# Kernel optimization log

Hardware: AMD Instinct MI355X
Metric: run time of the kernel (lower is better)

Reference implementation:

```python
import jax, jax.numpy as jnp
import numpy as np
import math

B, S, IN_DIM, OUT_DIM = 16, 1024, 512, 256
THETA = 10000.0


def _rope_single(x, cos, sin):
    # x: [B,S,D]; cos/sin: [D//2] -- SAME rotation applied at every position
    # (faithful to original: freqs_cis[seq_len*2] selects a single row)
    xr = x.reshape(x.shape[0], x.shape[1], -1, 2)
    a, b = xr[..., 0], xr[..., 1]
    out = jnp.stack([a * cos - b * sin, a * sin + b * cos], axis=-1)
    return out.reshape(x.shape)


def setup_inputs() -> dict:
    key = jax.random.key(0)
    ks = jax.random.split(key, 4)
    scale = 1.0 / math.sqrt(IN_DIM)
    x = jax.random.normal(ks[0], (B, S, IN_DIM), jnp.float32)
    wq = jax.random.normal(ks[1], (OUT_DIM, IN_DIM), jnp.float32) * scale
    wk = jax.random.normal(ks[2], (OUT_DIM, IN_DIM), jnp.float32) * scale
    wv = jax.random.normal(ks[3], (OUT_DIM, IN_DIM), jnp.float32) * scale
    bq = jnp.zeros((OUT_DIM,), jnp.float32)
    bk = jnp.zeros((OUT_DIM,), jnp.float32)
    bv = jnp.zeros((OUT_DIM,), jnp.float32)
    return {"x": x, "wq": wq, "bq": bq, "wk": wk, "bk": bk, "wv": wv, "bv": bv}


def reference(x, wq, bq, wk, bk, wv, bv):
    dim = x.shape[-1]  # scale uses INPUT dim, per original code
    # freqs_cis row at position index = 2*seq_len
    inv_freq = 1.0 / (THETA ** (jnp.arange(0, OUT_DIM, 2, dtype=jnp.float32) / OUT_DIM))
    angle = (2.0 * S) * inv_freq  # [OUT_DIM//2]
    cos, sin = jnp.cos(angle), jnp.sin(angle)

    q = jnp.einsum('bsi,oi->bso', x, wq) + bq
    k = jnp.einsum('bsi,oi->bso', x, wk) + bk
    v = jnp.einsum('bsi,oi->bso', x, wv) + bv

    q = _rope_single(q, cos, sin)
    k = _rope_single(k, cos, sin)

    scores = jnp.einsum('bqd,bkd->bqk', q, k) / jnp.sqrt(jnp.float32(dim))
    scores = jax.nn.softmax(scores.astype(jnp.float32), axis=-1)
    out = jnp.einsum('bqk,bkd->bqd', scores, v)
    return out
```

## Files before the change

### kernel.cpp

```cpp
#include <hip/hip_runtime.h>
#include <hip/hip_bf16.h>


typedef __attribute__((ext_vector_type(8))) short short8;
typedef __attribute__((ext_vector_type(4))) short short4v;
typedef __attribute__((ext_vector_type(4))) float f32x4;

#define GLL16(g, l)                                                            \
  __builtin_amdgcn_global_load_lds(                                            \
      (const __attribute__((address_space(1))) unsigned int*)(g),              \
      (__attribute__((address_space(3))) unsigned int*)(l), 16, 0, 0)

static __device__ __forceinline__ short f2bf(float f) {
  __hip_bfloat16 h = __float2bfloat16(f);
  return __builtin_bit_cast(short, h);
}

__global__ __launch_bounds__(256) void qkv_gemm(
    const float* __restrict__ x, const float* __restrict__ wq,
    const float* __restrict__ wk, const float* __restrict__ wv,
    const float* __restrict__ bq, const float* __restrict__ bk,
    const float* __restrict__ bv, short* __restrict__ qb,
    short* __restrict__ kb, short* __restrict__ vt) {
  __shared__ __align__(16) char smem[32768];
  const int bid = blockIdx.x;
  const int swz = (bid & 7) * 96 + (bid >> 3);
  const int mt = swz / 6, nt = swz % 6;
  const int tid = threadIdx.x;
  const int w = tid >> 6, lane = tid & 63;
  const int g = lane >> 4, c = lane & 15;
  const int wm = w >> 1, wn = w & 1;

  const float* wsel = (nt < 2) ? wq : (nt < 4) ? wk : wv;
  const int wro = (nt & 1) * 128;

  f32x4 acc[4][4];
  const f32x4 fzero = {0.f, 0.f, 0.f, 0.f};
#pragma unroll
  for (int mi = 0; mi < 4; mi++)
#pragma unroll
    for (int ni = 0; ni < 4; ni++) acc[mi][ni] = fzero;

  const int arow = tid >> 4;
  const int acol4 = tid & 15;
  const int achunk = acol4 >> 1, ahalf = (tid & 1) * 8;

  for (int kk = 0; kk < 8; ++kk) {
    __syncthreads();
    float4 xv[8], wv8[8];
#pragma unroll
    for (int j = 0; j < 8; j++) {
      int row = j * 16 + arow;
      xv[j] = *(const float4*)(x + (mt * 128 + row) * 512 + kk * 64 + acol4 * 4);
    }
#pragma unroll
    for (int j = 0; j < 8; j++) {
      int row = j * 16 + arow;
      wv8[j] = *(const float4*)(wsel + (wro + row) * 512 + kk * 64 + acol4 * 4);
    }
#pragma unroll
    for (int j = 0; j < 8; j++) {
      int row = j * 16 + arow;
      short4v s4;
      s4[0] = f2bf(xv[j].x); s4[1] = f2bf(xv[j].y);
      s4[2] = f2bf(xv[j].z); s4[3] = f2bf(xv[j].w);
      *(short4v*)(smem + row * 128 + ((achunk ^ (row & 7)) * 16) + ahalf) = s4;
      short4v t4;
      t4[0] = f2bf(wv8[j].x); t4[1] = f2bf(wv8[j].y);
      t4[2] = f2bf(wv8[j].z); t4[3] = f2bf(wv8[j].w);
      *(short4v*)(smem + 16384 + row * 128 + ((achunk ^ (row & 7)) * 16) + ahalf) = t4;
    }
    __syncthreads();
#pragma unroll
    for (int ks = 0; ks < 2; ++ks) {
      short8 af[4], bf[4];
#pragma unroll
      for (int mi = 0; mi < 4; mi++) {
        int row = wm * 64 + mi * 16 + c;
        af[mi] = *(const short8*)(smem + row * 128 + (((ks * 4 + g) ^ (row & 7)) * 16));
      }
#pragma unroll
      for (int ni = 0; ni < 4; ni++) {
        int row = wn * 64 + ni * 16 + c;
        bf[ni] = *(const short8*)(smem + 16384 + row * 128 + (((ks * 4 + g) ^ (row & 7)) * 16));
      }
#pragma unroll
      for (int mi = 0; mi < 4; mi++)
#pragma unroll
        for (int ni = 0; ni < 4; ni++)
          acc[mi][ni] = __builtin_amdgcn_mfma_f32_16x16x32_bf16(af[mi], bf[ni], acc[mi][ni], 0, 0, 0);
    }
  }

  const int cls = nt >> 1;
  const int cw = (nt & 1) * 128 + wn * 64;
  const int rowbase = mt * 128 + wm * 64;
  if (cls == 0) {
#pragma unroll
    for (int ni = 0; ni < 4; ni++) {
      int col = cw + ni * 16 + c;
      float bias = bq[col];
#pragma unroll
      for (int mi = 0; mi < 4; mi++)
#pragma unroll
        for (int j = 0; j < 4; j++) {
          int row = rowbase + mi * 16 + g * 4 + j;
          qb[row * 256 + col] = f2bf((acc[mi][ni][j] + bias) * 0.044194173824159216f);
        }
    }
  } else if (cls == 1) {
#pragma unroll
    for (int ni = 0; ni < 4; ni++) {
      int col = cw + ni * 16 + c;
      float bias = bk[col];
#pragma unroll
      for (int mi = 0; mi < 4; mi++)
#pragma unroll
        for (int j = 0; j < 4; j++) {
          int row = rowbase + mi * 16 + g * 4 + j;
          kb[row * 256 + col] = f2bf(acc[mi][ni][j] + bias);
        }
    }
  } else {
    __syncthreads();
    char* tb = smem + w * 8192;
#pragma unroll
    for (int ni = 0; ni < 4; ni++) {
      int dl = ni * 16 + c;
      float bias = bv[cw + dl];
#pragma unroll
      for (int mi = 0; mi < 4; mi++)
#pragma unroll
        for (int j = 0; j < 4; j++) {
          int sl = mi * 16 + g * 4 + j;
          *(short*)(tb + dl * 128 + ((sl * 2) ^ ((dl & 7) << 4))) =
              f2bf(acc[mi][ni][j] + bias);
        }
    }
    const int bb = rowbase >> 10, sb = rowbase & 1023;
#pragma unroll
    for (int i = 0; i < 8; i++) {
      int dl = i * 8 + (lane >> 3);
      int ch = lane & 7;
      short8 val = *(const short8*)(tb + dl * 128 + ((ch ^ (dl & 7)) * 16));
      *(short8*)(vt + (bb * 256 + cw + dl) * 1024 + sb + ch * 8) = val;
    }
  }
}

__global__ __launch_bounds__(512) void attn_kernel(
    const short* __restrict__ qb, const short* __restrict__ kb,
    const short* __restrict__ vt, float* __restrict__ out) {
  __shared__ __align__(16) char smem[149504];
  const int bid = blockIdx.x;
  const int swz = (bid & 7) * 32 + (bid >> 3);
  const int b = swz >> 4, qt = swz & 15;
  const int tid = threadIdx.x;
  const int w = tid >> 6, lane = tid & 63;
  const int grp = w >> 2, lw = w & 3;
  const int g = lane >> 4, c = lane & 15;
  const int q0 = b * 1024 + qt * 64 + lw * 16;
  char* kbase = smem + grp * 32768;
  char* vbase = smem + 65536 + grp * 32768;
  short* sp = (short*)(smem + 131072 + w * 2304);

  short8 qf[8];
#pragma unroll
  for (int ks = 0; ks < 8; ks++)
    qf[ks] = *(const short8*)(qb + (q0 + c) * 256 + ks * 32 + g * 8);

  f32x4 O[16];
  const f32x4 fzero = {0.f, 0.f, 0.f, 0.f};
#pragma unroll
  for (int ni = 0; ni < 16; ni++) O[ni] = fzero;
  float m_[4] = {-1e30f, -1e30f, -1e30f, -1e30f};
  float l_[4] = {0.f, 0.f, 0.f, 0.f};

  const int krow0 = b * 1024 + grp * 512;

  for (int kt = 0; kt < 8; ++kt) {
    __syncthreads();
    if (lw < 2) {
#pragma unroll
      for (int i = 0; i < 16; i++) {
        int j = lw * 16 + i;
        int r = j * 2 + (lane >> 5);
        int cc = lane & 31;
        GLL16(kb + (krow0 + kt * 64 + r) * 256 + ((cc ^ (r & 7)) * 8),
              kbase + j * 1024);
      }
    } else {
#pragma unroll
      for (int i = 0; i < 16; i++) {
        int j = (lw - 2) * 16 + i;
        int r = j * 8 + (lane >> 3);
        int cc = lane & 7;
        GLL16(vt + (b * 256 + r) * 1024 + grp * 512 + kt * 64 + ((cc ^ (r & 7)) * 8),
              vbase + j * 1024);
      }
    }
    asm volatile("s_waitcnt vmcnt(0)" ::: "memory");
    __syncthreads();

    f32x4 Sf[4];
#pragma unroll
    for (int nf = 0; nf < 4; nf++) Sf[nf] = fzero;
#pragma unroll
    for (int ks = 0; ks < 8; ks++) {
      short8 kf[4];
#pragma unroll
      for (int nf = 0; nf < 4; nf++) {
        int key = nf * 16 + c;
        kf[nf] = *(const short8*)(kbase + key * 512 + (((ks * 4 + g) ^ (c & 7)) * 16));
      }
#pragma unroll
      for (int nf = 0; nf < 4; nf++)
        Sf[nf] = __builtin_amdgcn_mfma_f32_16x16x32_bf16(qf[ks], kf[nf], Sf[nf], 0, 0, 0);
    }

    float Pv[4][4], scl[4];
#pragma unroll
    for (int j = 0; j < 4; j++) {
      float tm = fmaxf(fmaxf(Sf[0][j], Sf[1][j]), fmaxf(Sf[2][j], Sf[3][j]));
      tm = fmaxf(tm, __shfl_xor(tm, 1));
      tm = fmaxf(tm, __shfl_xor(tm, 2));
      tm = fmaxf(tm, __shfl_xor(tm, 4));
      tm = fmaxf(tm, __shfl_xor(tm, 8));
      float nm = fmaxf(m_[j], tm);
      scl[j] = __expf(m_[j] - nm);
      m_[j] = nm;
      float rs = 0.f;
#pragma unroll
      for (int nf = 0; nf < 4; nf++) {
        float p = __expf(Sf[nf][j] - nm);
        Pv[nf][j] = p;
        rs += p;
      }
      rs += __shfl_xor(rs, 1);
      rs += __shfl_xor(rs, 2);
      rs += __shfl_xor(rs, 4);
      rs += __shfl_xor(rs, 8);
      l_[j] = l_[j] * scl[j] + rs;
    }
#pragma unroll
    for (int ni = 0; ni < 16; ni++) {
      O[ni][0] *= scl[0]; O[ni][1] *= scl[1];
      O[ni][2] *= scl[2]; O[ni][3] *= scl[3];
    }

#pragma unroll
    for (int nf = 0; nf < 4; nf++)
#pragma unroll
      for (int j = 0; j < 4; j++)
        sp[(g * 4 + j) * 72 + nf * 16 + c] = f2bf(Pv[nf][j]);

    short8 pf[2];
#pragma unroll
    for (int ks2 = 0; ks2 < 2; ks2++)
      pf[ks2] = *(const short8*)((char*)sp + c * 144 + ks2 * 64 + g * 16);

#pragma unroll
    for (int ni = 0; ni < 16; ni++) {
      int d = ni * 16 + c;
#pragma unroll
      for (int ks2 = 0; ks2 < 2; ks2++) {
        short8 vf = *(const short8*)(vbase + d * 128 + (((ks2 * 4 + g) ^ (c & 7)) * 16));
        O[ni] = __builtin_amdgcn_mfma_f32_16x16x32_bf16(pf[ks2], vf, O[ni], 0, 0, 0);
      }
    }
  }

  __syncthreads();
  if (grp == 1) {
    char* ob = smem + lw * 20480;
#pragma unroll
    for (int ni = 0; ni < 16; ni++)
      *(f32x4*)(ob + (ni * 16 + c) * 80 + g * 16) = O[ni];
    float2* mlb = (float2*)(smem + 131072);
#pragma unroll
    for (int j = 0; j < 4; j++) {
      float2 ml; ml.x = m_[j]; ml.y = l_[j];
      mlb[lw * 16 + g * 4 + j] = ml;
    }
  }
  __syncthreads();
  if (grp == 0) {
    char* ob = smem + lw * 20480;
    const float2* mlb = (const float2*)(smem + 131072);
    float a1[4], a2[4], inv[4];
#pragma unroll
    for (int j = 0; j < 4; j++) {
      float2 ml2 = mlb[lw * 16 + g * 4 + j];
      float mm = fmaxf(m_[j], ml2.x);
      a1[j] = __expf(m_[j] - mm);
      a2[j] = __expf(ml2.x - mm);
      float l = a1[j] * l_[j] + a2[j] * ml2.y;
      inv[j] = 1.0f / l;
    }
#pragma unroll
    for (int ni = 0; ni < 16; ni++) {
      f32x4 o2 = *(const f32x4*)(ob + (ni * 16 + c) * 80 + g * 16);
#pragma unroll
      for (int j = 0; j < 4; j++) {
        int row = q0 + g * 4 + j;
        out[row * 256 + ni * 16 + c] = (a1[j] * O[ni][j] + a2[j] * o2[j]) * inv[j];
      }
    }
  }
}

extern "C" void kernel_launch(void* const* d_in, const int* in_sizes, int n_in,
                              void* d_out, int out_size, void* d_ws, size_t ws_size,
                              hipStream_t stream) {
  const float* x  = (const float*)d_in[0];
  const float* wq = (const float*)d_in[1];
  const float* bq = (const float*)d_in[2];
  const float* wk = (const float*)d_in[3];
  const float* bk = (const float*)d_in[4];
  const float* wv = (const float*)d_in[5];
  const float* bv = (const float*)d_in[6];
  float* out = (float*)d_out;
  char* ws = (char*)d_ws;
  short* qb = (short*)ws;
  short* kb = (short*)(ws + 8388608);
  short* vt = (short*)(ws + 16777216);

  qkv_gemm<<<768, 256, 0, stream>>>(x, wq, wk, wv, bq, bk, bv, qb, kb, vt);
  attn_kernel<<<256, 512, 0, stream>>>(qb, kb, vt, out);
}
```

Baseline: 156.3 us.

## Prefetch GEMM tiles, double-buffer K, read V from global, lazy softmax rescale

In the QKV GEMM, the next k-slice of x and W is loaded into registers while MFMAs run on the current LDS tile. In attention, K tiles are double-buffered in LDS and the next tile is issued before compute. V fragments are read straight from global memory into registers instead of being staged through LDS. The online softmax skips rescaling O unless the running max grows by more than 8. Launch bounds now request 2 blocks per CU, which caps registers and may cause spills. Uncoalesced per-lane global V reads could also add latency.

```diff
diff --git a/kernel.cpp b/kernel.cpp
--- a/kernel.cpp
+++ b/kernel.cpp
@@ -45,19 +45,16 @@
   const int acol4 = tid & 15;
   const int achunk = acol4 >> 1, ahalf = (tid & 1) * 8;
 
+  float4 xv[8], wv8[8];
+#pragma unroll
+  for (int j = 0; j < 8; j++) {
+    int row = j * 16 + arow;
+    xv[j] = *(const float4*)(x + (mt * 128 + row) * 512 + acol4 * 4);
+    wv8[j] = *(const float4*)(wsel + (wro + row) * 512 + acol4 * 4);
+  }
+
   for (int kk = 0; kk < 8; ++kk) {
     __syncthreads();
-    float4 xv[8], wv8[8];
-#pragma unroll
-    for (int j = 0; j < 8; j++) {
-      int row = j * 16 + arow;
-      xv[j] = *(const float4*)(x + (mt * 128 + row) * 512 + kk * 64 + acol4 * 4);
-    }
-#pragma unroll
-    for (int j = 0; j < 8; j++) {
-      int row = j * 16 + arow;
-      wv8[j] = *(const float4*)(wsel + (wro + row) * 512 + kk * 64 + acol4 * 4);
-    }
 #pragma unroll
     for (int j = 0; j < 8; j++) {
       int row = j * 16 + arow;
@@ -71,6 +68,14 @@
       *(short4v*)(smem + 16384 + row * 128 + ((achunk ^ (row & 7)) * 16) + ahalf) = t4;
     }
     __syncthreads();
+    if (kk < 7) {
+#pragma unroll
+      for (int j = 0; j < 8; j++) {
+        int row = j * 16 + arow;
+        xv[j] = *(const float4*)(x + (mt * 128 + row) * 512 + (kk + 1) * 64 + acol4 * 4);
+        wv8[j] = *(const float4*)(wsel + (wro + row) * 512 + (kk + 1) * 64 + acol4 * 4);
+      }
+    }
 #pragma unroll
     for (int ks = 0; ks < 2; ++ks) {
       short8 af[4], bf[4];
@@ -148,10 +153,10 @@
   }
 }
 
-__global__ __launch_bounds__(512) void attn_kernel(
+__global__ __launch_bounds__(512, 2) void attn_kernel(
     const short* __restrict__ qb, const short* __restrict__ kb,
     const short* __restrict__ vt, float* __restrict__ out) {
-  __shared__ __align__(16) char smem[149504];
+  __shared__ __align__(16) char smem[150016];
   const int bid = blockIdx.x;
   const int swz = (bid & 7) * 32 + (bid >> 3);
   const int b = swz >> 4, qt = swz & 15;
@@ -160,9 +165,9 @@
   const int grp = w >> 2, lw = w & 3;
   const int g = lane >> 4, c = lane & 15;
   const int q0 = b * 1024 + qt * 64 + lw * 16;
-  char* kbase = smem + grp * 32768;
-  char* vbase = smem + 65536 + grp * 32768;
   short* sp = (short*)(smem + 131072 + w * 2304);
+  const int krow0 = b * 1024 + grp * 512;
+  const short* vrow = vt + (size_t)(b * 256) * 1024 + grp * 512;
 
   short8 qf[8];
 #pragma unroll
@@ -176,31 +181,25 @@
   float m_[4] = {-1e30f, -1e30f, -1e30f, -1e30f};
   float l_[4] = {0.f, 0.f, 0.f, 0.f};
 
-  const int krow0 = b * 1024 + grp * 512;
-
+  auto stageK = [&](int kt, int buf) {
+    char* dst = smem + (grp * 2 + buf) * 32768;
+#pragma unroll
+    for (int i = 0; i < 8; i++) {
+      int j = lw * 8 + i;
+      int r = j * 2 + (lane >> 5);
+      int cc = lane & 31;
+      GLL16(kb + (krow0 + kt * 64 + r) * 256 + ((cc ^ (r & 7)) * 8),
+            dst + j * 1024);
+    }
+  };
+
+  stageK(0, 0);
   for (int kt = 0; kt < 8; ++kt) {
-    __syncthreads();
-    if (lw < 2) {
-#pragma unroll
-      for (int i = 0; i < 16; i++) {
-        int j = lw * 16 + i;
-        int r = j * 2 + (lane >> 5);
-        int cc = lane & 31;
-        GLL16(kb + (krow0 + kt * 64 + r) * 256 + ((cc ^ (r & 7)) * 8),
-              kbase + j * 1024);
-      }
-    } else {
-#pragma unroll
-      for (int i = 0; i < 16; i++) {
-        int j = (lw - 2) * 16 + i;
-        int r = j * 8 + (lane >> 3);
-        int cc = lane & 7;
-        GLL16(vt + (b * 256 + r) * 1024 + grp * 512 + kt * 64 + ((cc ^ (r & 7)) * 8),
-              vbase + j * 1024);
-      }
-    }
+    const int cur = kt & 1;
+    const char* kbase = smem + (grp * 2 + cur) * 32768;
     asm volatile("s_waitcnt vmcnt(0)" ::: "memory");
     __syncthreads();
+    if (kt < 7) stageK(kt + 1, cur ^ 1);
 
     f32x4 Sf[4];
 #pragma unroll
@@ -218,34 +217,65 @@
         Sf[nf] = __builtin_amdgcn_mfma_f32_16x16x32_bf16(qf[ks], kf[nf], Sf[nf], 0, 0, 0);
     }
 
-    float Pv[4][4], scl[4];
+    short8 vfA[16];
+#pragma unroll
+    for (int ni = 0; ni < 16; ni++)
+      vfA[ni] = *(const short8*)(vrow + (size_t)(ni * 16 + c) * 1024 + kt * 64 + g * 8);
+
+    float tm[4];
 #pragma unroll
     for (int j = 0; j < 4; j++) {
-      float tm = fmaxf(fmaxf(Sf[0][j], Sf[1][j]), fmaxf(Sf[2][j], Sf[3][j]));
-      tm = fmaxf(tm, __shfl_xor(tm, 1));
-      tm = fmaxf(tm, __shfl_xor(tm, 2));
-      tm = fmaxf(tm, __shfl_xor(tm, 4));
-      tm = fmaxf(tm, __shfl_xor(tm, 8));
-      float nm = fmaxf(m_[j], tm);
-      scl[j] = __expf(m_[j] - nm);
-      m_[j] = nm;
-      float rs = 0.f;
-#pragma unroll
-      for (int nf = 0; nf < 4; nf++) {
-        float p = __expf(Sf[nf][j] - nm);
-        Pv[nf][j] = p;
-        rs += p;
-      }
-      rs += __shfl_xor(rs, 1);
-      rs += __shfl_xor(rs, 2);
-      rs += __shfl_xor(rs, 4);
-      rs += __shfl_xor(rs, 8);
-      l_[j] = l_[j] * scl[j] + rs;
-    }
-#pragma unroll
-    for (int ni = 0; ni < 16; ni++) {
-      O[ni][0] *= scl[0]; O[ni][1] *= scl[1];
-      O[ni][2] *= scl[2]; O[ni][3] *= scl[3];
+      float t = fmaxf(fmaxf(Sf[0][j], Sf[1][j]), fmaxf(Sf[2][j], Sf[3][j]));
+      t = fmaxf(t, __shfl_xor(t, 1));
+      t = fmaxf(t, __shfl_xor(t, 2));
+      t = fmaxf(t, __shfl_xor(t, 4));
+      t = fmaxf(t, __shfl_xor(t, 8));
+      tm[j] = t;
+    }
+    bool need = (tm[0] > m_[0] + 8.f) || (tm[1] > m_[1] + 8.f) ||
+                (tm[2] > m_[2] + 8.f) || (tm[3] > m_[3] + 8.f);
+    float Pv[4][4];
+    if (__any(need)) {
+      float scl[4];
+#pragma unroll
+      for (int j = 0; j < 4; j++) {
+        float nm = fmaxf(m_[j], tm[j]);
+        scl[j] = __expf(m_[j] - nm);
+        m_[j] = nm;
+        float rs = 0.f;
+#pragma unroll
+        for (int nf = 0; nf < 4; nf++) {
+          float p = __expf(Sf[nf][j] - nm);
+          Pv[nf][j] = p;
+          rs += p;
+        }
+        rs += __shfl_xor(rs, 1);
+        rs += __shfl_xor(rs, 2);
+        rs += __shfl_xor(rs, 4);
+        rs += __shfl_xor(rs, 8);
+        l_[j] = l_[j] * scl[j] + rs;
+      }
+#pragma unroll
+      for (int ni = 0; ni < 16; ni++) {
+        O[ni][0] *= scl[0]; O[ni][1] *= scl[1];
+        O[ni][2] *= scl[2]; O[ni][3] *= scl[3];
+      }
+    } else {
+#pragma unroll
+      for (int j = 0; j < 4; j++) {
+        float rs = 0.f;
+#pragma unroll
+        for (int nf = 0; nf < 4; nf++) {
+          float p = __expf(Sf[nf][j] - m_[j]);
+          Pv[nf][j] = p;
+          rs += p;
+        }
+        rs += __shfl_xor(rs, 1);
+        rs += __shfl_xor(rs, 2);
+        rs += __shfl_xor(rs, 4);
+        rs += __shfl_xor(rs, 8);
+        l_[j] += rs;
+      }
     }
 
 #pragma unroll
@@ -260,23 +290,24 @@
       pf[ks2] = *(const short8*)((char*)sp + c * 144 + ks2 * 64 + g * 16);
 
 #pragma unroll
-    for (int ni = 0; ni < 16; ni++) {
-      int d = ni * 16 + c;
-#pragma unroll
-      for (int ks2 = 0; ks2 < 2; ks2++) {
-        short8 vf = *(const short8*)(vbase + d * 128 + (((ks2 * 4 + g) ^ (c & 7)) * 16));
-        O[ni] = __builtin_amdgcn_mfma_f32_16x16x32_bf16(pf[ks2], vf, O[ni], 0, 0, 0);
-      }
-    }
+    for (int ni = 0; ni < 16; ni++)
+      O[ni] = __builtin_amdgcn_mfma_f32_16x16x32_bf16(pf[0], vfA[ni], O[ni], 0, 0, 0);
+    short8 vfB[16];
+#pragma unroll
+    for (int ni = 0; ni < 16; ni++)
+      vfB[ni] = *(const short8*)(vrow + (size_t)(ni * 16 + c) * 1024 + kt * 64 + 32 + g * 8);
+#pragma unroll
+    for (int ni = 0; ni < 16; ni++)
+      O[ni] = __builtin_amdgcn_mfma_f32_16x16x32_bf16(pf[1], vfB[ni], O[ni], 0, 0, 0);
   }
 
   __syncthreads();
+  float2* mlb = (float2*)(smem + 149504);
   if (grp == 1) {
     char* ob = smem + lw * 20480;
 #pragma unroll
     for (int ni = 0; ni < 16; ni++)
       *(f32x4*)(ob + (ni * 16 + c) * 80 + g * 16) = O[ni];
-    float2* mlb = (float2*)(smem + 131072);
 #pragma unroll
     for (int j = 0; j < 4; j++) {
       float2 ml; ml.x = m_[j]; ml.y = l_[j];
@@ -286,7 +317,6 @@
   __syncthreads();
   if (grp == 0) {
     char* ob = smem + lw * 20480;
-    const float2* mlb = (const float2*)(smem + 131072);
     float a1[4], a2[4], inv[4];
 #pragma unroll
     for (int j = 0; j < 4; j++) {
@@ -294,8 +324,7 @@
       float mm = fmaxf(m_[j], ml2.x);
       a1[j] = __expf(m_[j] - mm);
       a2[j] = __expf(ml2.x - mm);
-      float l = a1[j] * l_[j] + a2[j] * ml2.y;
-      inv[j] = 1.0f / l;
+      inv[j] = 1.0f / (a1[j] * l_[j] + a2[j] * ml2.y);
     }
 #pragma unroll
     for (int ni = 0; ni < 16; ni++) {
```

Result: slower. 294.0 us (+88.1%).
